# Optimization experiments

Measured on AMD Instinct MI355X. Metric: run time of the kernel, lower is better.

Reference implementation:

```python
import jax, jax.numpy as jnp
import numpy as np

N = 50000          # nodes
E = 1600000        # edges (before self-loops)
IN = 512           # in_channels
H = 8              # heads
C1 = 8             # per-head channels of conv1 (== heads)
OUT = 64           # out_channels
SLOPE = 0.2        # GATConv leaky_relu negative slope


def setup_inputs() -> dict:
    key = jax.random.key(0)
    ks = jax.random.split(key, 10)
    x = jax.random.normal(ks[0], (N, IN), jnp.float32)
    edge_index = jax.random.randint(ks[1], (2, E), 0, N, dtype=jnp.int64)
    s1 = 1.0 / np.sqrt(IN)
    s2 = 1.0 / np.sqrt(H * C1)
    W1 = jax.random.normal(ks[2], (IN, H * C1), jnp.float32) * s1
    att_src1 = jax.random.normal(ks[3], (H, C1), jnp.float32) * s2
    att_dst1 = jax.random.normal(ks[4], (H, C1), jnp.float32) * s2
    b1 = jnp.zeros((H * C1,), jnp.float32)
    W2 = jax.random.normal(ks[5], (H * C1, OUT), jnp.float32) * s2
    att_src2 = jax.random.normal(ks[6], (1, OUT), jnp.float32) * 0.1
    att_dst2 = jax.random.normal(ks[7], (1, OUT), jnp.float32) * 0.1
    b2 = jnp.zeros((OUT,), jnp.float32)
    return {"x": x, "edge_index": edge_index, "W1": W1, "att_src1": att_src1,
            "att_dst1": att_dst1, "b1": b1, "W2": W2, "att_src2": att_src2,
            "att_dst2": att_dst2, "b2": b2}


def gat_layer(x, src, dst, W, a_src, a_dst, b, heads, ch, concat):
    n = x.shape[0]
    h = (x @ W).reshape(n, heads, ch)                       # [N,H,C]
    alpha_src = jnp.einsum('nhc,hc->nh', h, a_src)          # [N,H]
    alpha_dst = jnp.einsum('nhc,hc->nh', h, a_dst)
    e = jax.nn.leaky_relu(alpha_src[src] + alpha_dst[dst], SLOPE)  # [Etot,H]
    # segment softmax over incoming edges of each destination node
    m = jax.ops.segment_max(e, dst, num_segments=n)
    ex = jnp.exp(e - m[dst])
    denom = jax.ops.segment_sum(ex, dst, num_segments=n)
    alpha = ex / (denom[dst] + 1e-16)                       # [Etot,H]
    out = jax.ops.segment_sum(h[src] * alpha[:, :, None], dst, num_segments=n)
    out = out.reshape(n, heads * ch) if concat else out.mean(axis=1)
    return out + b


def reference(x, edge_index, W1, att_src1, att_dst1, b1, W2, att_src2, att_dst2, b2):
    n = x.shape[0]
    loops = jnp.arange(n, dtype=edge_index.dtype)           # add_self_loops=True
    src = jnp.concatenate([edge_index[0], loops])
    dst = jnp.concatenate([edge_index[1], loops])
    h = jax.nn.elu(gat_layer(x, src, dst, W1, att_src1, att_dst1, b1, H, C1, True))
    # F.dropout in eval mode is identity
    out = gat_layer(h, src, dst, W2, att_src2, att_dst2, b2, 1, OUT, False)
    return jax.nn.log_softmax(out, axis=-1)
```

## Files before the change

### kernel.cpp

```cpp
#include <hip/hip_runtime.h>
#include <hip/hip_bf16.h>
#include <math.h>


#define WAVE 64
#define NPB_SHIFT 7
#define NB_MAX 512
#define NBLK 128
#define CAP 6144

typedef __attribute__((ext_vector_type(8))) short short8;
typedef __attribute__((ext_vector_type(4))) float f32x4;

__device__ inline float wred_sum(float v) {
#pragma unroll
    for (int off = 32; off > 0; off >>= 1) v += __shfl_xor(v, off);
    return v;
}
__device__ inline float wred_max(float v) {
#pragma unroll
    for (int off = 32; off > 0; off >>= 1) v = fmaxf(v, __shfl_xor(v, off));
    return v;
}
__device__ inline unsigned short f2bf(float f) {
    unsigned u = __float_as_uint(f);
    u += 0x7FFFu + ((u >> 16) & 1u);
    return (unsigned short)(u >> 16);
}

__global__ __launch_bounds__(256) void bucket_count(const int* __restrict__ ei,
                                                    int* __restrict__ hist,
                                                    int E, int Et, int NB, int epb) {
    __shared__ int lh[NB_MAX];
    for (int t = threadIdx.x; t < NB; t += 256) lh[t] = 0;
    __syncthreads();
    int e0 = blockIdx.x * epb;
    int e1 = min(e0 + epb, Et);
    for (int e = e0 + threadIdx.x; e < e1; e += 256) {
        int d = (e < E) ? ei[E + e] : (e - E);
        atomicAdd(&lh[d >> NPB_SHIFT], 1);
    }
    __syncthreads();
    for (int t = threadIdx.x; t < NB; t += 256)
        hist[blockIdx.x * NB + t] = lh[t];
}

__global__ __launch_bounds__(512) void bucket_scan(int* __restrict__ hist,
                                                   int* __restrict__ bBase,
                                                   int* __restrict__ rowptr,
                                                   int NB, int nblk, int n) {
    __shared__ int tot[NB_MAX];
    for (int b = threadIdx.x; b < NB; b += 512) {
        int s = 0;
        for (int j = 0; j < nblk; ++j) s += hist[j * NB + b];
        tot[b] = s;
    }
    __syncthreads();
    if (threadIdx.x == 0) {
        int run = 0;
        for (int b = 0; b < NB; ++b) { int t = tot[b]; tot[b] = run; bBase[b] = run; run += t; }
        bBase[NB] = run;
        rowptr[n] = run;
    }
    __syncthreads();
    for (int b = threadIdx.x; b < NB; b += 512) {
        int run = tot[b];
        for (int j = 0; j < nblk; ++j) { int t = hist[j * NB + b]; hist[j * NB + b] = run; run += t; }
    }
}

__global__ __launch_bounds__(256) void bucket_scatter(const int* __restrict__ ei,
                                                      const int* __restrict__ hist,
                                                      unsigned* __restrict__ region,
                                                      int E, int Et, int NB, int epb) {
    __shared__ int gb[NB_MAX];
    __shared__ int off[NB_MAX];
    for (int t = threadIdx.x; t < NB; t += 256) { gb[t] = hist[blockIdx.x * NB + t]; off[t] = 0; }
    __syncthreads();
    int e0 = blockIdx.x * epb;
    int e1 = min(e0 + epb, Et);
    for (int e = e0 + threadIdx.x; e < e1; e += 256) {
        int s, d;
        if (e < E) { s = ei[e]; d = ei[E + e]; }
        else       { s = d = e - E; }
        int b = d >> NPB_SHIFT;
        int p = gb[b] + atomicAdd(&off[b], 1);
        region[p] = (unsigned)s | ((unsigned)(d & 127) << 16);
    }
}

__global__ __launch_bounds__(256) void bucket_build(unsigned* __restrict__ region,
                                                    const int* __restrict__ bBase,
                                                    int* __restrict__ rowptr, int n) {
    __shared__ int deg[128], rp[129], cur[128];
    __shared__ unsigned short sb[CAP];
    int b = blockIdx.x;
    int base = bBase[b];
    int cnt  = min(bBase[b + 1] - base, CAP);
    int tid  = threadIdx.x;
    if (tid < 128) { deg[tid] = 0; cur[tid] = 0; }
    __syncthreads();
    for (int i = tid; i < cnt; i += 256)
        atomicAdd(&deg[region[base + i] >> 16], 1);
    __syncthreads();
    if (tid == 0) {
        int run = 0;
        for (int t = 0; t < 128; ++t) { rp[t] = run; run += deg[t]; }
        rp[128] = run;
    }
    __syncthreads();
    int nodeLo = b << NPB_SHIFT;
    if (tid < 128 && nodeLo + tid < n) rowptr[nodeLo + tid] = base + rp[tid];
    for (int i = tid; i < cnt; i += 256) {
        unsigned v = region[base + i];
        int dl = v >> 16;
        int p = rp[dl] + atomicAdd(&cur[dl], 1);
        sb[p] = (unsigned short)(v & 0xFFFFu);
    }
    __syncthreads();
    for (int i = tid; i < cnt; i += 256)
        region[base + i] = (unsigned)sb[i];
}

__global__ __launch_bounds__(256) void wtrans_kernel(const float* __restrict__ W,
                                                     unsigned short* __restrict__ wtg) {
    int idx = blockIdx.x * 256 + threadIdx.x;
    if (idx >= 64 * 512) return;
    int c = idx >> 9, k = idx & 511;
    wtg[c * 512 + k] = f2bf(W[k * 64 + c]);
}

__global__ __launch_bounds__(256) void gemm1_mfma(const float* __restrict__ X,
                                                  const unsigned short* __restrict__ wtg,
                                                  float* __restrict__ O, int nrows) {
    __shared__ unsigned short xs[64][40];
    __shared__ unsigned short wt[64][40];
    int tid  = threadIdx.x;
    int wid  = tid >> 6;
    int lane = tid & 63;
    int lr   = lane & 15;
    int lg   = lane >> 4;
    int bm   = blockIdx.x * 64;

    f32x4 acc[4];
#pragma unroll
    for (int i = 0; i < 4; ++i) acc[i] = (f32x4){0.f, 0.f, 0.f, 0.f};

    for (int k0 = 0; k0 < 512; k0 += 32) {
#pragma unroll
        for (int i = 0; i < 2; ++i) {
            int p = tid + i * 256;
            int row = p >> 3, c4 = p & 7;
            float4 v = {0.f, 0.f, 0.f, 0.f};
            if (bm + row < nrows)
                v = *(const float4*)(X + (size_t)(bm + row) * 512 + k0 + c4 * 4);
            unsigned short* dst = &xs[row][c4 * 4];
            dst[0] = f2bf(v.x); dst[1] = f2bf(v.y); dst[2] = f2bf(v.z); dst[3] = f2bf(v.w);
        }
        {
            int c = tid >> 2, kq = tid & 3;
            *(short8*)&wt[c][kq * 8] = *(const short8*)&wtg[c * 512 + k0 + kq * 8];
        }
        __syncthreads();
        short8 af = *(short8*)&xs[wid * 16 + lr][lg * 8];
#pragma unroll
        for (int cb = 0; cb < 4; ++cb) {
            short8 bfb = *(short8*)&wt[cb * 16 + lr][lg * 8];
            acc[cb] = __builtin_amdgcn_mfma_f32_16x16x32_bf16(af, bfb, acc[cb], 0, 0, 0);
        }
        __syncthreads();
    }
#pragma unroll
    for (int cb = 0; cb < 4; ++cb)
#pragma unroll
        for (int r = 0; r < 4; ++r) {
            int m = bm + wid * 16 + lg * 4 + r;
            if (m < nrows) O[(size_t)m * 64 + cb * 16 + lr] = acc[cb][r];
        }
}

__global__ __launch_bounds__(256) void gemm64(const float* __restrict__ X,
                                              const float* __restrict__ W,
                                              float* __restrict__ O, int nrows, int K) {
    __shared__ float xs[32][68];
    __shared__ float ws[32][68];
    int tid = threadIdx.x;
    int bm = blockIdx.x * 64;
    int tx = tid & 15;
    int ty = tid >> 4;
    float acc[4][4] = {{0.f}};
    for (int k0 = 0; k0 < K; k0 += 32) {
#pragma unroll
        for (int i = 0; i < 2; ++i) {
            int p = tid + i * 256;
            int row = p >> 3, k4 = p & 7;
            float4 v = {0.f, 0.f, 0.f, 0.f};
            if (bm + row < nrows)
                v = *(const float4*)(X + (size_t)(bm + row) * K + k0 + k4 * 4);
            xs[k4 * 4 + 0][row] = v.x; xs[k4 * 4 + 1][row] = v.y;
            xs[k4 * 4 + 2][row] = v.z; xs[k4 * 4 + 3][row] = v.w;
        }
#pragma unroll
        for (int i = 0; i < 2; ++i) {
            int p = tid + i * 256;
            int kr = p >> 4, c4 = p & 15;
            float4 v = *(const float4*)(W + (size_t)(k0 + kr) * 64 + c4 * 4);
            ws[kr][c4 * 4 + 0] = v.x; ws[kr][c4 * 4 + 1] = v.y;
            ws[kr][c4 * 4 + 2] = v.z; ws[kr][c4 * 4 + 3] = v.w;
        }
        __syncthreads();
#pragma unroll
        for (int kk = 0; kk < 32; ++kk) {
            float a[4], bq[4];
#pragma unroll
            for (int i = 0; i < 4; ++i) a[i] = xs[kk][ty * 4 + i];
#pragma unroll
            for (int j = 0; j < 4; ++j) bq[j] = ws[kk][tx * 4 + j];
#pragma unroll
            for (int i = 0; i < 4; ++i)
#pragma unroll
                for (int j = 0; j < 4; ++j) acc[i][j] = fmaf(a[i], bq[j], acc[i][j]);
        }
        __syncthreads();
    }
    int row0 = bm + ty * 4;
#pragma unroll
    for (int i = 0; i < 4; ++i) {
        int r = row0 + i;
        if (r < nrows) {
            float4 v = {acc[i][0], acc[i][1], acc[i][2], acc[i][3]};
            *(float4*)(O + (size_t)r * 64 + tx * 4) = v;
        }
    }
}

__global__ __launch_bounds__(256) void alpha1_kernel(const float* __restrict__ H1,
                                                     const float* __restrict__ as1,
                                                     const float* __restrict__ ad1,
                                                     float* __restrict__ asrc,
                                                     float* __restrict__ adst, int n) {
    int idx = blockIdx.x * 256 + threadIdx.x;
    if (idx >= n * 8) return;
    int h = idx & 7;
    const float* hp = H1 + (size_t)(idx >> 3) * 64 + h * 8;
    float s = 0.f, d = 0.f;
#pragma unroll
    for (int c = 0; c < 8; ++c) {
        float v = hp[c];
        s = fmaf(v, as1[h * 8 + c], s);
        d = fmaf(v, ad1[h * 8 + c], d);
    }
    asrc[idx] = s;
    adst[idx] = d;
}

__global__ __launch_bounds__(256) void alpha2_kernel(const float* __restrict__ H2,
                                                     const float* __restrict__ as2,
                                                     const float* __restrict__ ad2,
                                                     float* __restrict__ asrc,
                                                     float* __restrict__ adst, int n) {
    int node = blockIdx.x * 4 + (threadIdx.x >> 6);
    int lane = threadIdx.x & 63;
    if (node >= n) return;
    float v = H2[(size_t)node * 64 + lane];
    float s = wred_sum(v * as2[lane]);
    float d = wred_sum(v * ad2[lane]);
    if (lane == 0) { asrc[node] = s; adst[node] = d; }
}

__global__ __launch_bounds__(256) void agg1_kernel(const float* __restrict__ H1,
                                                   const float* __restrict__ asrc,
                                                   const float* __restrict__ adst,
                                                   const int* __restrict__ rowptr,
                                                   const int* __restrict__ csrc,
                                                   const float* __restrict__ b1,
                                                   float* __restrict__ out1, int n) {
    __shared__ float wbuf[4][64][8];
    __shared__ int   sbuf[4][64];
    int wid  = threadIdx.x >> 6;
    int lane = threadIdx.x & 63;
    int node = blockIdx.x * 4 + wid;
    if (node >= n) return;
    int h = lane >> 3;
    int beg = rowptr[node], end = rowptr[node + 1];

    float ad[8];
    *(float4*)&ad[0] = *(const float4*)&adst[(size_t)node * 8];
    *(float4*)&ad[4] = *(const float4*)&adst[(size_t)node * 8 + 4];

    float lsum[8];
#pragma unroll
    for (int i = 0; i < 8; ++i) lsum[i] = 0.f;
    float acc0 = 0.f, acc1 = 0.f;

    for (int c0 = beg; c0 < end; c0 += 64) {
        int e = c0 + lane;
        if (e < end) {
            int s = csrc[e];
            sbuf[wid][lane] = s;
            float a[8], p[8];
            *(float4*)&a[0] = *(const float4*)&asrc[(size_t)s * 8];
            *(float4*)&a[4] = *(const float4*)&asrc[(size_t)s * 8 + 4];
#pragma unroll
            for (int i = 0; i < 8; ++i) {
                float t = a[i] + ad[i];
                t = t > 0.f ? t : 0.2f * t;
                p[i] = __expf(t);
                lsum[i] += p[i];
            }
            *(float4*)&wbuf[wid][lane][0] = *(float4*)&p[0];
            *(float4*)&wbuf[wid][lane][4] = *(float4*)&p[4];
        }
        int cnt = min(64, end - c0);
        int i = 0;
        for (; i + 3 < cnt; i += 4) {
            int s0 = sbuf[wid][i + 0], s1 = sbuf[wid][i + 1];
            int s2 = sbuf[wid][i + 2], s3 = sbuf[wid][i + 3];
            float w0 = wbuf[wid][i + 0][h], w1 = wbuf[wid][i + 1][h];
            float w2 = wbuf[wid][i + 2][h], w3 = wbuf[wid][i + 3][h];
            float g0 = H1[(size_t)s0 * 64 + lane];
            float g1 = H1[(size_t)s1 * 64 + lane];
            float g2 = H1[(size_t)s2 * 64 + lane];
            float g3 = H1[(size_t)s3 * 64 + lane];
            acc0 = fmaf(g0, w0, acc0);
            acc1 = fmaf(g1, w1, acc1);
            acc0 = fmaf(g2, w2, acc0);
            acc1 = fmaf(g3, w3, acc1);
        }
        for (; i < cnt; ++i) {
            int s   = sbuf[wid][i];
            float w = wbuf[wid][i][h];
            acc0 = fmaf(H1[(size_t)s * 64 + lane], w, acc0);
        }
    }
    float acc = acc0 + acc1;
#pragma unroll
    for (int off = 32; off > 0; off >>= 1)
#pragma unroll
        for (int i = 0; i < 8; ++i) lsum[i] += __shfl_xor(lsum[i], off);
    float L = lsum[0];
#pragma unroll
    for (int i = 1; i < 8; ++i) if (h == i) L = lsum[i];
    float o = acc / (L + 1e-16f) + b1[lane];
    out1[(size_t)node * 64 + lane] = o > 0.f ? o : expm1f(o);
}

__global__ __launch_bounds__(256) void agg2_kernel(const float* __restrict__ H2,
                                                   const float* __restrict__ asrc,
                                                   const float* __restrict__ adst,
                                                   const int* __restrict__ rowptr,
                                                   const int* __restrict__ csrc,
                                                   const float* __restrict__ b2,
                                                   float* __restrict__ out, int n) {
    __shared__ float wbuf[4][64];
    __shared__ int   sbuf[4][64];
    int wid  = threadIdx.x >> 6;
    int lane = threadIdx.x & 63;
    int node = blockIdx.x * 4 + wid;
    if (node >= n) return;
    int beg = rowptr[node], end = rowptr[node + 1];
    float ad = adst[node];

    float lsum = 0.f, acc0 = 0.f, acc1 = 0.f;
    for (int c0 = beg; c0 < end; c0 += 64) {
        int e = c0 + lane;
        if (e < end) {
            int s = csrc[e];
            sbuf[wid][lane] = s;
            float t = asrc[s] + ad;
            t = t > 0.f ? t : 0.2f * t;
            float p = __expf(t);
            lsum += p;
            wbuf[wid][lane] = p;
        }
        int cnt = min(64, end - c0);
        int i = 0;
        for (; i + 3 < cnt; i += 4) {
            int s0 = sbuf[wid][i + 0], s1 = sbuf[wid][i + 1];
            int s2 = sbuf[wid][i + 2], s3 = sbuf[wid][i + 3];
            float w0 = wbuf[wid][i + 0], w1 = wbuf[wid][i + 1];
            float w2 = wbuf[wid][i + 2], w3 = wbuf[wid][i + 3];
            float g0 = H2[(size_t)s0 * 64 + lane];
            float g1 = H2[(size_t)s1 * 64 + lane];
            float g2 = H2[(size_t)s2 * 64 + lane];
            float g3 = H2[(size_t)s3 * 64 + lane];
            acc0 = fmaf(g0, w0, acc0);
            acc1 = fmaf(g1, w1, acc1);
            acc0 = fmaf(g2, w2, acc0);
            acc1 = fmaf(g3, w3, acc1);
        }
        for (; i < cnt; ++i) {
            acc0 = fmaf(H2[(size_t)sbuf[wid][i] * 64 + lane], wbuf[wid][i], acc0);
        }
    }
    lsum = wred_sum(lsum);
    float o = (acc0 + acc1) / (lsum + 1e-16f) + b2[lane];
    float mx = wred_max(o);
    float se = wred_sum(__expf(o - mx));
    out[(size_t)node * 64 + lane] = o - mx - logf(se);
}

extern "C" void kernel_launch(void* const* d_in, const int* in_sizes, int n_in,
                              void* d_out, int out_size, void* d_ws, size_t ws_size,
                              hipStream_t stream) {
    const float* x   = (const float*)d_in[0];
    const int*   ei  = (const int*)d_in[1];
    const float* W1  = (const float*)d_in[2];
    const float* as1 = (const float*)d_in[3];
    const float* ad1 = (const float*)d_in[4];
    const float* b1  = (const float*)d_in[5];
    const float* W2  = (const float*)d_in[6];
    const float* as2 = (const float*)d_in[7];
    const float* ad2 = (const float*)d_in[8];
    const float* b2  = (const float*)d_in[9];
    float* out = (float*)d_out;

    const int n  = in_sizes[0] / 512;
    const int E  = in_sizes[1] / 2;
    const int Et = E + n;
    const int NB  = (n + 127) >> NPB_SHIFT;
    const int epb = (Et + NBLK - 1) / NBLK;

    char* w = (char*)d_ws;
    auto alloc = [&](size_t bytes) {
        char* p = w;
        w += (bytes + 255) & ~(size_t)255;
        return p;
    };
    int*            hist   = (int*)alloc((size_t)NBLK * NB * 4);
    int*            bBase  = (int*)alloc((size_t)(NB + 1) * 4);
    unsigned*       region = (unsigned*)alloc((size_t)Et * 4);
    int*            rowptr = (int*)alloc((size_t)(n + 1) * 4);
    float*          h1     = (float*)alloc((size_t)n * 64 * 4);
    float*          out1   = (float*)alloc((size_t)n * 64 * 4);
    float*          h2     = (float*)alloc((size_t)n * 64 * 4);
    float*          asrc1  = (float*)alloc((size_t)n * 8 * 4);
    float*          adst1  = (float*)alloc((size_t)n * 8 * 4);
    float*          asrc2  = (float*)alloc((size_t)n * 4);
    float*          adst2  = (float*)alloc((size_t)n * 4);
    unsigned short* wtg    = (unsigned short*)alloc((size_t)64 * 512 * 2);
    int*            csrc   = (int*)region;

    bucket_count  <<<NBLK, 256, 0, stream>>>(ei, hist, E, Et, NB, epb);
    bucket_scan   <<<1,    512, 0, stream>>>(hist, bBase, rowptr, NB, NBLK, n);
    bucket_scatter<<<NBLK, 256, 0, stream>>>(ei, hist, region, E, Et, NB, epb);
    bucket_build  <<<NB,   256, 0, stream>>>(region, bBase, rowptr, n);

    wtrans_kernel<<<(64 * 512 + 255) / 256, 256, 0, stream>>>(W1, wtg);
    gemm1_mfma<<<(n + 63) / 64, 256, 0, stream>>>(x, wtg, h1, n);
    alpha1_kernel<<<(n * 8 + 255) / 256, 256, 0, stream>>>(h1, as1, ad1, asrc1, adst1, n);
    agg1_kernel<<<(n + 3) / 4, 256, 0, stream>>>(h1, asrc1, adst1, rowptr, csrc, b1, out1, n);

    gemm64<<<(n + 63) / 64, 256, 0, stream>>>(out1, W2, h2, n, 64);
    alpha2_kernel<<<(n + 3) / 4, 256, 0, stream>>>(h2, as2, ad2, asrc2, adst2, n);
    agg2_kernel<<<(n + 3) / 4, 256, 0, stream>>>(h2, asrc2, adst2, rowptr, csrc, b2, out, n);
}
```

Baseline: 440.5 us.

## Store node features in bf16 and use MFMA for second-layer GEMM

Intermediate node feature tensors (h1, out1, h2) and the per-node source attention logits of layer 1 are now stored as bf16 instead of fp32, roughly halving the bytes moved by the edge-gather aggregation kernels. The fp32 scalar-FMA gemm64 for layer 2 is replaced by a bf16 MFMA kernel, with an added kernel that transposes W2 into bf16. Accumulation stays in fp32, but the extra rounding of activations and attention logits may reduce accuracy relative to the fp32 reference.

```diff
diff --git a/kernel.cpp b/kernel.cpp
--- a/kernel.cpp
+++ b/kernel.cpp
@@ -26,6 +26,9 @@
     unsigned u = __float_as_uint(f);
     u += 0x7FFFu + ((u >> 16) & 1u);
     return (unsigned short)(u >> 16);
+}
+__device__ inline float bf2f(unsigned short u) {
+    return __uint_as_float((unsigned)u << 16);
 }
 
 __global__ __launch_bounds__(256) void bucket_count(const int* __restrict__ ei,
@@ -130,9 +133,17 @@
     wtg[c * 512 + k] = f2bf(W[k * 64 + c]);
 }
 
+__global__ __launch_bounds__(256) void wtrans2_kernel(const float* __restrict__ W,
+                                                      unsigned short* __restrict__ wt2) {
+    int idx = blockIdx.x * 256 + threadIdx.x;
+    if (idx >= 64 * 64) return;
+    int c = idx >> 6, k = idx & 63;
+    wt2[c * 64 + k] = f2bf(W[k * 64 + c]);
+}
+
 __global__ __launch_bounds__(256) void gemm1_mfma(const float* __restrict__ X,
                                                   const unsigned short* __restrict__ wtg,
-                                                  float* __restrict__ O, int nrows) {
+                                                  unsigned short* __restrict__ O, int nrows) {
     __shared__ unsigned short xs[64][40];
     __shared__ unsigned short wt[64][40];
     int tid  = threadIdx.x;
@@ -175,86 +186,79 @@
 #pragma unroll
         for (int r = 0; r < 4; ++r) {
             int m = bm + wid * 16 + lg * 4 + r;
-            if (m < nrows) O[(size_t)m * 64 + cb * 16 + lr] = acc[cb][r];
-        }
-}
-
-__global__ __launch_bounds__(256) void gemm64(const float* __restrict__ X,
-                                              const float* __restrict__ W,
-                                              float* __restrict__ O, int nrows, int K) {
-    __shared__ float xs[32][68];
-    __shared__ float ws[32][68];
-    int tid = threadIdx.x;
-    int bm = blockIdx.x * 64;
-    int tx = tid & 15;
-    int ty = tid >> 4;
-    float acc[4][4] = {{0.f}};
-    for (int k0 = 0; k0 < K; k0 += 32) {
-#pragma unroll
-        for (int i = 0; i < 2; ++i) {
-            int p = tid + i * 256;
-            int row = p >> 3, k4 = p & 7;
-            float4 v = {0.f, 0.f, 0.f, 0.f};
+            if (m < nrows) O[(size_t)m * 64 + cb * 16 + lr] = f2bf(acc[cb][r]);
+        }
+}
+
+__global__ __launch_bounds__(256) void gemm2_mfma(const unsigned short* __restrict__ X,
+                                                  const unsigned short* __restrict__ wt2,
+                                                  unsigned short* __restrict__ O, int nrows) {
+    __shared__ unsigned short xs[64][40];
+    __shared__ unsigned short wt[64][40];
+    int tid  = threadIdx.x;
+    int wid  = tid >> 6;
+    int lane = tid & 63;
+    int lr   = lane & 15;
+    int lg   = lane >> 4;
+    int bm   = blockIdx.x * 64;
+
+    f32x4 acc[4];
+#pragma unroll
+    for (int i = 0; i < 4; ++i) acc[i] = (f32x4){0.f, 0.f, 0.f, 0.f};
+
+#pragma unroll
+    for (int k0 = 0; k0 < 64; k0 += 32) {
+        {
+            int row = tid >> 2, kq = tid & 3;
+            short8 v = {0, 0, 0, 0, 0, 0, 0, 0};
             if (bm + row < nrows)
-                v = *(const float4*)(X + (size_t)(bm + row) * K + k0 + k4 * 4);
-            xs[k4 * 4 + 0][row] = v.x; xs[k4 * 4 + 1][row] = v.y;
-            xs[k4 * 4 + 2][row] = v.z; xs[k4 * 4 + 3][row] = v.w;
-        }
-#pragma unroll
-        for (int i = 0; i < 2; ++i) {
-            int p = tid + i * 256;
-            int kr = p >> 4, c4 = p & 15;
-            float4 v = *(const float4*)(W + (size_t)(k0 + kr) * 64 + c4 * 4);
-            ws[kr][c4 * 4 + 0] = v.x; ws[kr][c4 * 4 + 1] = v.y;
-            ws[kr][c4 * 4 + 2] = v.z; ws[kr][c4 * 4 + 3] = v.w;
+                v = *(const short8*)&X[(size_t)(bm + row) * 64 + k0 + kq * 8];
+            *(short8*)&xs[row][kq * 8] = v;
+        }
+        {
+            int c = tid >> 2, kq = tid & 3;
+            *(short8*)&wt[c][kq * 8] = *(const short8*)&wt2[c * 64 + k0 + kq * 8];
         }
         __syncthreads();
-#pragma unroll
-        for (int kk = 0; kk < 32; ++kk) {
-            float a[4], bq[4];
-#pragma unroll
-            for (int i = 0; i < 4; ++i) a[i] = xs[kk][ty * 4 + i];
-#pragma unroll
-            for (int j = 0; j < 4; ++j) bq[j] = ws[kk][tx * 4 + j];
-#pragma unroll
-            for (int i = 0; i < 4; ++i)
-#pragma unroll
-                for (int j = 0; j < 4; ++j) acc[i][j] = fmaf(a[i], bq[j], acc[i][j]);
+        short8 af = *(short8*)&xs[wid * 16 + lr][lg * 8];
+#pragma unroll
+        for (int cb = 0; cb < 4; ++cb) {
+            short8 bfb = *(short8*)&wt[cb * 16 + lr][lg * 8];
+            acc[cb] = __builtin_amdgcn_mfma_f32_16x16x32_bf16(af, bfb, acc[cb], 0, 0, 0);
         }
         __syncthreads();
     }
-    int row0 = bm + ty * 4;
-#pragma unroll
-    for (int i = 0; i < 4; ++i) {
-        int r = row0 + i;
-        if (r < nrows) {
-            float4 v = {acc[i][0], acc[i][1], acc[i][2], acc[i][3]};
-            *(float4*)(O + (size_t)r * 64 + tx * 4) = v;
-        }
-    }
-}
-
-__global__ __launch_bounds__(256) void alpha1_kernel(const float* __restrict__ H1,
+#pragma unroll
+    for (int cb = 0; cb < 4; ++cb)
+#pragma unroll
+        for (int r = 0; r < 4; ++r) {
+            int m = bm + wid * 16 + lg * 4 + r;
+            if (m < nrows) O[(size_t)m * 64 + cb * 16 + lr] = f2bf(acc[cb][r]);
+        }
+}
+
+__global__ __launch_bounds__(256) void alpha1_kernel(const unsigned short* __restrict__ H1b,
                                                      const float* __restrict__ as1,
                                                      const float* __restrict__ ad1,
-                                                     float* __restrict__ asrc,
+                                                     unsigned short* __restrict__ asrc,
                                                      float* __restrict__ adst, int n) {
     int idx = blockIdx.x * 256 + threadIdx.x;
     if (idx >= n * 8) return;
     int h = idx & 7;
-    const float* hp = H1 + (size_t)(idx >> 3) * 64 + h * 8;
+    const unsigned short* hp = H1b + (size_t)(idx >> 3) * 64 + h * 8;
+    short8 hv = *(const short8*)hp;
     float s = 0.f, d = 0.f;
 #pragma unroll
     for (int c = 0; c < 8; ++c) {
-        float v = hp[c];
+        float v = bf2f((unsigned short)hv[c]);
         s = fmaf(v, as1[h * 8 + c], s);
         d = fmaf(v, ad1[h * 8 + c], d);
     }
-    asrc[idx] = s;
+    asrc[idx] = f2bf(s);
     adst[idx] = d;
 }
 
-__global__ __launch_bounds__(256) void alpha2_kernel(const float* __restrict__ H2,
+__global__ __launch_bounds__(256) void alpha2_kernel(const unsigned short* __restrict__ H2b,
                                                      const float* __restrict__ as2,
                                                      const float* __restrict__ ad2,
                                                      float* __restrict__ asrc,
@@ -262,19 +266,19 @@
     int node = blockIdx.x * 4 + (threadIdx.x >> 6);
     int lane = threadIdx.x & 63;
     if (node >= n) return;
-    float v = H2[(size_t)node * 64 + lane];
+    float v = bf2f(H2b[(size_t)node * 64 + lane]);
     float s = wred_sum(v * as2[lane]);
     float d = wred_sum(v * ad2[lane]);
     if (lane == 0) { asrc[node] = s; adst[node] = d; }
 }
 
-__global__ __launch_bounds__(256) void agg1_kernel(const float* __restrict__ H1,
-                                                   const float* __restrict__ asrc,
+__global__ __launch_bounds__(256) void agg1_kernel(const unsigned short* __restrict__ H1b,
+                                                   const unsigned short* __restrict__ asrc,
                                                    const float* __restrict__ adst,
                                                    const int* __restrict__ rowptr,
                                                    const int* __restrict__ csrc,
                                                    const float* __restrict__ b1,
-                                                   float* __restrict__ out1, int n) {
+                                                   unsigned short* __restrict__ out1, int n) {
     __shared__ float wbuf[4][64][8];
     __shared__ int   sbuf[4][64];
     int wid  = threadIdx.x >> 6;
@@ -298,12 +302,11 @@
         if (e < end) {
             int s = csrc[e];
             sbuf[wid][lane] = s;
-            float a[8], p[8];
-            *(float4*)&a[0] = *(const float4*)&asrc[(size_t)s * 8];
-            *(float4*)&a[4] = *(const float4*)&asrc[(size_t)s * 8 + 4];
+            short8 av = *(const short8*)&asrc[(size_t)s * 8];
+            float p[8];
 #pragma unroll
             for (int i = 0; i < 8; ++i) {
-                float t = a[i] + ad[i];
+                float t = bf2f((unsigned short)av[i]) + ad[i];
                 t = t > 0.f ? t : 0.2f * t;
                 p[i] = __expf(t);
                 lsum[i] += p[i];
@@ -318,10 +321,10 @@
             int s2 = sbuf[wid][i + 2], s3 = sbuf[wid][i + 3];
             float w0 = wbuf[wid][i + 0][h], w1 = wbuf[wid][i + 1][h];
             float w2 = wbuf[wid][i + 2][h], w3 = wbuf[wid][i + 3][h];
-            float g0 = H1[(size_t)s0 * 64 + lane];
-            float g1 = H1[(size_t)s1 * 64 + lane];
-            float g2 = H1[(size_t)s2 * 64 + lane];
-            float g3 = H1[(size_t)s3 * 64 + lane];
+            float g0 = bf2f(H1b[(size_t)s0 * 64 + lane]);
+            float g1 = bf2f(H1b[(size_t)s1 * 64 + lane]);
+            float g2 = bf2f(H1b[(size_t)s2 * 64 + lane]);
+            float g3 = bf2f(H1b[(size_t)s3 * 64 + lane]);
             acc0 = fmaf(g0, w0, acc0);
             acc1 = fmaf(g1, w1, acc1);
             acc0 = fmaf(g2, w2, acc0);
@@ -330,7 +333,7 @@
         for (; i < cnt; ++i) {
             int s   = sbuf[wid][i];
             float w = wbuf[wid][i][h];
-            acc0 = fmaf(H1[(size_t)s * 64 + lane], w, acc0);
+            acc0 = fmaf(bf2f(H1b[(size_t)s * 64 + lane]), w, acc0);
         }
     }
     float acc = acc0 + acc1;
@@ -342,10 +345,11 @@
 #pragma unroll
     for (int i = 1; i < 8; ++i) if (h == i) L = lsum[i];
     float o = acc / (L + 1e-16f) + b1[lane];
-    out1[(size_t)node * 64 + lane] = o > 0.f ? o : expm1f(o);
-}
-
-__global__ __launch_bounds__(256) void agg2_kernel(const float* __restrict__ H2,
+    o = o > 0.f ? o : expm1f(o);
+    out1[(size_t)node * 64 + lane] = f2bf(o);
+}
+
+__global__ __launch_bounds__(256) void agg2_kernel(const unsigned short* __restrict__ H2b,
                                                    const float* __restrict__ asrc,
                                                    const float* __restrict__ adst,
                                                    const int* __restrict__ rowptr,
@@ -380,17 +384,17 @@
             int s2 = sbuf[wid][i + 2], s3 = sbuf[wid][i + 3];
             float w0 = wbuf[wid][i + 0], w1 = wbuf[wid][i + 1];
             float w2 = wbuf[wid][i + 2], w3 = wbuf[wid][i + 3];
-            float g0 = H2[(size_t)s0 * 64 + lane];
-            float g1 = H2[(size_t)s1 * 64 + lane];
-            float g2 = H2[(size_t)s2 * 64 + lane];
-            float g3 = H2[(size_t)s3 * 64 + lane];
+            float g0 = bf2f(H2b[(size_t)s0 * 64 + lane]);
+            float g1 = bf2f(H2b[(size_t)s1 * 64 + lane]);
+            float g2 = bf2f(H2b[(size_t)s2 * 64 + lane]);
+            float g3 = bf2f(H2b[(size_t)s3 * 64 + lane]);
             acc0 = fmaf(g0, w0, acc0);
             acc1 = fmaf(g1, w1, acc1);
             acc0 = fmaf(g2, w2, acc0);
             acc1 = fmaf(g3, w3, acc1);
         }
         for (; i < cnt; ++i) {
-            acc0 = fmaf(H2[(size_t)sbuf[wid][i] * 64 + lane], wbuf[wid][i], acc0);
+            acc0 = fmaf(bf2f(H2b[(size_t)sbuf[wid][i] * 64 + lane]), wbuf[wid][i], acc0);
         }
     }
     lsum = wred_sum(lsum);
@@ -431,14 +435,15 @@
     int*            bBase  = (int*)alloc((size_t)(NB + 1) * 4);
     unsigned*       region = (unsigned*)alloc((size_t)Et * 4);
     int*            rowptr = (int*)alloc((size_t)(n + 1) * 4);
-    float*          h1     = (float*)alloc((size_t)n * 64 * 4);
-    float*          out1   = (float*)alloc((size_t)n * 64 * 4);
-    float*          h2     = (float*)alloc((size_t)n * 64 * 4);
-    float*          asrc1  = (float*)alloc((size_t)n * 8 * 4);
+    unsigned short* h1b    = (unsigned short*)alloc((size_t)n * 64 * 2);
+    unsigned short* out1b  = (unsigned short*)alloc((size_t)n * 64 * 2);
+    unsigned short* h2b    = (unsigned short*)alloc((size_t)n * 64 * 2);
+    unsigned short* asrc1b = (unsigned short*)alloc((size_t)n * 8 * 2);
     float*          adst1  = (float*)alloc((size_t)n * 8 * 4);
     float*          asrc2  = (float*)alloc((size_t)n * 4);
     float*          adst2  = (float*)alloc((size_t)n * 4);
     unsigned short* wtg    = (unsigned short*)alloc((size_t)64 * 512 * 2);
+    unsigned short* wtg2   = (unsigned short*)alloc((size_t)64 * 64 * 2);
     int*            csrc   = (int*)region;
 
     bucket_count  <<<NBLK, 256, 0, stream>>>(ei, hist, E, Et, NB, epb);
@@ -447,11 +452,12 @@
     bucket_build  <<<NB,   256, 0, stream>>>(region, bBase, rowptr, n);
 
     wtrans_kernel<<<(64 * 512 + 255) / 256, 256, 0, stream>>>(W1, wtg);
-    gemm1_mfma<<<(n + 63) / 64, 256, 0, stream>>>(x, wtg, h1, n);
-    alpha1_kernel<<<(n * 8 + 255) / 256, 256, 0, stream>>>(h1, as1, ad1, asrc1, adst1, n);
-    agg1_kernel<<<(n + 3) / 4, 256, 0, stream>>>(h1, asrc1, adst1, rowptr, csrc, b1, out1, n);
-
-    gemm64<<<(n + 63) / 64, 256, 0, stream>>>(out1, W2, h2, n, 64);
-    alpha2_kernel<<<(n + 3) / 4, 256, 0, stream>>>(h2, as2, ad2, asrc2, adst2, n);
-    agg2_kernel<<<(n + 3) / 4, 256, 0, stream>>>(h2, asrc2, adst2, rowptr, csrc, b2, out, n);
-}
+    gemm1_mfma<<<(n + 63) / 64, 256, 0, stream>>>(x, wtg, h1b, n);
+    alpha1_kernel<<<(n * 8 + 255) / 256, 256, 0, stream>>>(h1b, as1, ad1, asrc1b, adst1, n);
+    agg1_kernel<<<(n + 3) / 4, 256, 0, stream>>>(h1b, asrc1b, adst1, rowptr, csrc, b1, out1b, n);
+
+    wtrans2_kernel<<<(64 * 64 + 255) / 256, 256, 0, stream>>>(W2, wtg2);
+    gemm2_mfma<<<(n + 63) / 64, 256, 0, stream>>>(out1b, wtg2, h2b, n);
+    alpha2_kernel<<<(n + 3) / 4, 256, 0, stream>>>(h2b, as2, ad2, asrc2, adst2, n);
+    agg2_kernel<<<(n + 3) / 4, 256, 0, stream>>>(h2b, asrc2, adst2, rowptr, csrc, b2, out, n);
+}
```

Result: faster. 415.1 us (-5.8%).
